# Kernel tuning notes

Measured on AMD Instinct MI355X. Metric: run time of the kernel, lower is better.

## Reference

```python
import jax, jax.numpy as jnp
import numpy as np

N, M, D = 16384, 4096, 128
NEG = -1e30  # masked-score fill


def setup_inputs() -> dict:
    key = jax.random.key(0)
    k1, k2, k3, k4 = jax.random.split(key, 4)
    self_feats = jax.random.normal(k1, (N, D), dtype=jnp.float32)
    features_neighs = jax.random.normal(k2, (M, D), dtype=jnp.float32)
    neigh_matrix = jax.random.randint(k3, (N, M), 0, 2, dtype=jnp.int32)
    # xavier_uniform for a: shape (2D, 1), gain=1 -> limit = sqrt(6/(2D+1))
    limit = float(np.sqrt(6.0 / (2 * D + 1)))
    a = jax.random.uniform(k4, (2 * D, 1), minval=-limit, maxval=limit, dtype=jnp.float32)
    return {"self_feats": self_feats, "features_neighs": features_neighs,
            "neigh_matrix": neigh_matrix, "a": a}


def reference(self_feats, features_neighs, neigh_matrix, a):
    # a = [a_self; a_neigh]; cat([self_i, neigh_j]) @ a = self_i@a_self + neigh_j@a_neigh
    d = self_feats.shape[1]
    s_self = self_feats @ a[:d, 0]        # [N]
    s_neigh = features_neighs @ a[d:, 0]  # [M]
    scores = jax.nn.leaky_relu(s_self[:, None] + s_neigh[None, :], 0.2)  # [N, M]
    mask = neigh_matrix.astype(bool)
    scores = jnp.where(mask, scores, NEG)
    attn = jax.nn.softmax(scores, axis=1)          # masked softmax per node
    attn = jnp.where(mask, attn, 0.0)              # nodes with no neighbors -> zeros
    return attn @ features_neighs                  # [N, D] weighted neighbor sum
```

## Files before the change

### kernel.cpp

```cpp
#include <hip/hip_runtime.h>
#include <hip/hip_bf16.h>

#define NROWS 16384
#define MCOLS 4096
#define DDIM  128
#define LOG2E 1.4426950408889634f

typedef __attribute__((ext_vector_type(8))) short short8;
typedef __attribute__((ext_vector_type(4))) float f32x4;

__device__ __forceinline__ float wave_reduce_add(float d) {
#pragma unroll
  for (int off = 32; off >= 1; off >>= 1) d += __shfl_xor(d, off, 64);
  return d;
}

__device__ __forceinline__ float pcalc(float t, int m) {
  float u = fmaxf(t, 0.2f * t);
  float e = exp2f(u);
  return m != 0 ? e : 0.f;
}

__device__ __forceinline__ unsigned short f2bf(float f) {
  unsigned u = __builtin_bit_cast(unsigned, f);
  return (unsigned short)((u + 0x7fffu + ((u >> 16) & 1u)) >> 16);
}

__device__ __forceinline__ unsigned pack_bf2(float lo, float hi) {
  return (unsigned)f2bf(lo) | ((unsigned)f2bf(hi) << 16);
}

__global__ __launch_bounds__(256) void aggr_prep(
    const float* __restrict__ V, const float* __restrict__ a,
    float* __restrict__ sneigh, short* __restrict__ packedV) {
  const int t = threadIdx.x, lane = t & 63, w = t >> 6;
  const int blk = blockIdx.x;

  float a0 = a[DDIM + 2 * lane] * LOG2E;
  float a1 = a[DDIM + 2 * lane + 1] * LOG2E;
#pragma unroll
  for (int i = 0; i < 4; ++i) {
    int j = blk * 16 + w * 4 + i;
    float2 v = *(const float2*)(V + (long)j * DDIM + 2 * lane);
    float d = wave_reduce_add(v.x * a0 + v.y * a1);
    if (lane == 0) sneigh[j] = d;
  }

  const int tg = blk * 256 + t;
  const int l = tg & 63;
  const int chunkid = tg >> 6;
  const int c = chunkid & 15, kt = chunkid >> 4;
  const int ks2 = c >> 3, cf = c & 7;
  const int col = cf * 16 + (l & 15);
  const long krow = (long)kt * 64 + ks2 * 32 + (l >> 4) * 8;
  short8 o;
#pragma unroll
  for (int b = 0; b < 8; ++b) {
    float f = V[(krow + b) * DDIM + col];
    o[b] = (short)f2bf(f);
  }
  *(short8*)(packedV + (long)tg * 8) = o;
}

__global__ __launch_bounds__(512, 2) void aggr_main(
    const float* __restrict__ self_feats, const int* __restrict__ nm,
    const float* __restrict__ a, const float* __restrict__ sneigh,
    const short* __restrict__ packedV, float* __restrict__ out) {
  __shared__ float s_sn[MCOLS];
  __shared__ float s_ss[64];
  __shared__ __align__(16) short Bst[2][2][8192];
  __shared__ float comb[4][16][132];
  __shared__ float den_x[64];
  __shared__ float den_f[64];

  const int t = threadIdx.x, lane = t & 63, w = t >> 6;
  const int rw = w & 3, ks = w >> 2;
  const int blk = blockIdx.x;
  const int rowblk = blk * 64;
  const int arow = lane & 15, kg = lane >> 4;

  {
    float a0 = a[2 * lane] * LOG2E, a1 = a[2 * lane + 1] * LOG2E;
#pragma unroll
    for (int i = 0; i < 8; ++i) {
      int r = w * 8 + i;
      float2 v = *(const float2*)(self_feats + (long)(rowblk + r) * DDIM + 2 * lane);
      float d = wave_reduce_add(v.x * a0 + v.y * a1);
      if (lane == 0) s_ss[r] = d;
    }
  }
  {
    const float4* src = (const float4*)sneigh;
    float4* dst = (float4*)s_sn;
    dst[t] = src[t];
    dst[t + 512] = src[t + 512];
  }

  auto STAGE = [&](int buf, int it2) {
    int ktn = it2 * 2 + ks;
#pragma unroll
    for (int j = 0; j < 4; ++j) {
      int c = (w & 3) * 4 + j;
      const short* g = packedV + ((long)(ktn * 16 + c) * 64 + lane) * 8;
      __builtin_amdgcn_global_load_lds(
          (const __attribute__((address_space(1))) void*)g,
          (__attribute__((address_space(3))) void*)(&Bst[buf][ks][c * 512]),
          16, 0, 0);
    }
  };

  const int* mbase = nm + (long)(rowblk + rw * 16 + arow) * MCOLS + kg * 8;

  int4 mc[4], mn[4] = {};
  STAGE(0, 0);
  {
    const int kt0 = ks;
#pragma unroll
    for (int ks2 = 0; ks2 < 2; ++ks2)
#pragma unroll
      for (int q = 0; q < 2; ++q)
        mc[ks2 * 2 + q] = *(const int4*)(mbase + kt0 * 64 + ks2 * 32 + q * 4);
  }
  __syncthreads();

  const float si = s_ss[rw * 16 + arow];

  f32x4 acc[8];
#pragma unroll
  for (int i = 0; i < 8; ++i) acc[i] = (f32x4){0.f, 0.f, 0.f, 0.f};
  float den = 0.f;

#pragma unroll 2
  for (int it = 0; it < 32; ++it) {
    const int kt = it * 2 + ks;
    const int buf = it & 1;
    if (it < 31) {
      STAGE(buf ^ 1, it + 1);
      __builtin_amdgcn_sched_barrier(0);
      const int ktn = (it + 1) * 2 + ks;
#pragma unroll
      for (int ks2 = 0; ks2 < 2; ++ks2)
#pragma unroll
        for (int q = 0; q < 2; ++q)
          mn[ks2 * 2 + q] = *(const int4*)(mbase + ktn * 64 + ks2 * 32 + q * 4);
      __builtin_amdgcn_sched_barrier(0);
    }

    short8 afr[2];
#pragma unroll
    for (int ks2 = 0; ks2 < 2; ++ks2) {
      const float* sj = &s_sn[kt * 64 + ks2 * 32 + kg * 8];
      float4 s0 = *(const float4*)sj;
      float4 s1 = *(const float4*)(sj + 4);
      int4 m0 = mc[ks2 * 2], m1 = mc[ks2 * 2 + 1];
      float p0 = pcalc(si + s0.x, m0.x);
      float p1 = pcalc(si + s0.y, m0.y);
      float p2 = pcalc(si + s0.z, m0.z);
      float p3 = pcalc(si + s0.w, m0.w);
      float p4 = pcalc(si + s1.x, m1.x);
      float p5 = pcalc(si + s1.y, m1.y);
      float p6 = pcalc(si + s1.z, m1.z);
      float p7 = pcalc(si + s1.w, m1.w);
      den += ((p0 + p1) + (p2 + p3)) + ((p4 + p5) + (p6 + p7));
      int4 ai;
      ai.x = (int)pack_bf2(p0, p1);
      ai.y = (int)pack_bf2(p2, p3);
      ai.z = (int)pack_bf2(p4, p5);
      ai.w = (int)pack_bf2(p6, p7);
      afr[ks2] = __builtin_bit_cast(short8, ai);
    }

    const short8* Bks = (const short8*)&Bst[buf][ks][0];
#pragma unroll
    for (int cf = 0; cf < 8; ++cf) {
      acc[cf] = __builtin_amdgcn_mfma_f32_16x16x32_bf16(afr[0], Bks[cf * 64 + lane], acc[cf], 0, 0, 0);
      acc[cf] = __builtin_amdgcn_mfma_f32_16x16x32_bf16(afr[1], Bks[(8 + cf) * 64 + lane], acc[cf], 0, 0, 0);
    }

    asm volatile("s_waitcnt vmcnt(4)" ::: "memory");
    __builtin_amdgcn_sched_barrier(0);
    __builtin_amdgcn_s_barrier();
    mc[0] = mn[0]; mc[1] = mn[1]; mc[2] = mn[2]; mc[3] = mn[3];
  }

  den += __shfl_xor(den, 16, 64);
  den += __shfl_xor(den, 32, 64);

  if (ks == 1) {
#pragma unroll
    for (int cf = 0; cf < 8; ++cf)
#pragma unroll
      for (int r = 0; r < 4; ++r)
        comb[rw][kg * 4 + r][cf * 16 + arow] = acc[cf][r];
    if (lane < 16) den_x[rw * 16 + lane] = den;
  }
  __syncthreads();
  if (ks == 0) {
    float dtot = den + den_x[rw * 16 + arow];
    if (lane < 16) den_f[rw * 16 + lane] = dtot;
  }
  __syncthreads();
  if (ks == 0) {
    float rcp[4];
#pragma unroll
    for (int r = 0; r < 4; ++r) {
      float dv = den_f[rw * 16 + kg * 4 + r];
      rcp[r] = dv > 0.f ? 1.0f / dv : 0.f;
    }
#pragma unroll
    for (int cf = 0; cf < 8; ++cf)
#pragma unroll
      for (int r = 0; r < 4; ++r) {
        float v = (acc[cf][r] + comb[rw][kg * 4 + r][cf * 16 + arow]) * rcp[r];
        out[(long)(rowblk + rw * 16 + kg * 4 + r) * DDIM + cf * 16 + arow] = v;
      }
  }
}

extern "C" void kernel_launch(void* const* d_in, const int* in_sizes, int n_in,
                              void* d_out, int out_size, void* d_ws, size_t ws_size,
                              hipStream_t stream) {
  const float* self_feats = (const float*)d_in[0];
  const float* V = (const float*)d_in[1];
  const int* nm = (const int*)d_in[2];
  const float* a = (const float*)d_in[3];
  float* out = (float*)d_out;

  float* sneigh = (float*)d_ws;
  short* packedV = (short*)((char*)d_ws + 16384);

  aggr_prep<<<256, 256, 0, stream>>>(V, a, sneigh, packedV);
  aggr_main<<<256, 512, 0, stream>>>(self_feats, nm, a, sneigh, packedV, out);
}
```

Before: 400.5 us.

## Drop intra-block K split; use four waves each covering full K range

Removes the two-way split of the neighbor dimension across wave groups, so each of four waves processes all 64 K tiles for its 16 rows. This eliminates the LDS combine buffers, two block barriers and the cross-group partial-sum reduction. Block size drops from 512 to 256 threads while the grid stays at 256 blocks. The cost is that each CU has half as many waves issuing mask loads, which lowers memory-level parallelism in a bandwidth/latency bound loop.

```diff
diff --git a/kernel.cpp b/kernel.cpp
--- a/kernel.cpp
+++ b/kernel.cpp
@@ -62,19 +62,15 @@
   *(short8*)(packedV + (long)tg * 8) = o;
 }
 
-__global__ __launch_bounds__(512, 2) void aggr_main(
+__global__ __launch_bounds__(256, 3) void aggr_main(
     const float* __restrict__ self_feats, const int* __restrict__ nm,
     const float* __restrict__ a, const float* __restrict__ sneigh,
     const short* __restrict__ packedV, float* __restrict__ out) {
   __shared__ float s_sn[MCOLS];
   __shared__ float s_ss[64];
-  __shared__ __align__(16) short Bst[2][2][8192];
-  __shared__ float comb[4][16][132];
-  __shared__ float den_x[64];
-  __shared__ float den_f[64];
+  __shared__ __align__(16) short Bst[2][8192];
 
   const int t = threadIdx.x, lane = t & 63, w = t >> 6;
-  const int rw = w & 3, ks = w >> 2;
   const int blk = blockIdx.x;
   const int rowblk = blk * 64;
   const int arow = lane & 15, kg = lane >> 4;
@@ -82,8 +78,8 @@
   {
     float a0 = a[2 * lane] * LOG2E, a1 = a[2 * lane + 1] * LOG2E;
 #pragma unroll
-    for (int i = 0; i < 8; ++i) {
-      int r = w * 8 + i;
+    for (int i = 0; i < 16; ++i) {
+      int r = w * 16 + i;
       float2 v = *(const float2*)(self_feats + (long)(rowblk + r) * DDIM + 2 * lane);
       float d = wave_reduce_add(v.x * a0 + v.y * a1);
       if (lane == 0) s_ss[r] = d;
@@ -93,37 +89,35 @@
     const float4* src = (const float4*)sneigh;
     float4* dst = (float4*)s_sn;
     dst[t] = src[t];
+    dst[t + 256] = src[t + 256];
     dst[t + 512] = src[t + 512];
-  }
-
-  auto STAGE = [&](int buf, int it2) {
-    int ktn = it2 * 2 + ks;
+    dst[t + 768] = src[t + 768];
+  }
+
+  auto STAGE = [&](int buf, int kt) {
 #pragma unroll
     for (int j = 0; j < 4; ++j) {
-      int c = (w & 3) * 4 + j;
-      const short* g = packedV + ((long)(ktn * 16 + c) * 64 + lane) * 8;
+      int c = w * 4 + j;
+      const short* g = packedV + ((long)(kt * 16 + c) * 64 + lane) * 8;
       __builtin_amdgcn_global_load_lds(
           (const __attribute__((address_space(1))) void*)g,
-          (__attribute__((address_space(3))) void*)(&Bst[buf][ks][c * 512]),
+          (__attribute__((address_space(3))) void*)(&Bst[buf][c * 512]),
           16, 0, 0);
     }
   };
 
-  const int* mbase = nm + (long)(rowblk + rw * 16 + arow) * MCOLS + kg * 8;
+  const int* mbase = nm + (long)(rowblk + w * 16 + arow) * MCOLS + kg * 8;
 
   int4 mc[4], mn[4] = {};
   STAGE(0, 0);
-  {
-    const int kt0 = ks;
-#pragma unroll
-    for (int ks2 = 0; ks2 < 2; ++ks2)
-#pragma unroll
-      for (int q = 0; q < 2; ++q)
-        mc[ks2 * 2 + q] = *(const int4*)(mbase + kt0 * 64 + ks2 * 32 + q * 4);
-  }
+#pragma unroll
+  for (int ks2 = 0; ks2 < 2; ++ks2)
+#pragma unroll
+    for (int q = 0; q < 2; ++q)
+      mc[ks2 * 2 + q] = *(const int4*)(mbase + ks2 * 32 + q * 4);
   __syncthreads();
 
-  const float si = s_ss[rw * 16 + arow];
+  const float si = s_ss[w * 16 + arow];
 
   f32x4 acc[8];
 #pragma unroll
@@ -131,25 +125,23 @@
   float den = 0.f;
 
 #pragma unroll 2
-  for (int it = 0; it < 32; ++it) {
-    const int kt = it * 2 + ks;
+  for (int it = 0; it < 64; ++it) {
     const int buf = it & 1;
-    if (it < 31) {
+    if (it < 63) {
       STAGE(buf ^ 1, it + 1);
       __builtin_amdgcn_sched_barrier(0);
-      const int ktn = (it + 1) * 2 + ks;
 #pragma unroll
       for (int ks2 = 0; ks2 < 2; ++ks2)
 #pragma unroll
         for (int q = 0; q < 2; ++q)
-          mn[ks2 * 2 + q] = *(const int4*)(mbase + ktn * 64 + ks2 * 32 + q * 4);
+          mn[ks2 * 2 + q] = *(const int4*)(mbase + (it + 1) * 64 + ks2 * 32 + q * 4);
       __builtin_amdgcn_sched_barrier(0);
     }
 
     short8 afr[2];
 #pragma unroll
     for (int ks2 = 0; ks2 < 2; ++ks2) {
-      const float* sj = &s_sn[kt * 64 + ks2 * 32 + kg * 8];
+      const float* sj = &s_sn[it * 64 + ks2 * 32 + kg * 8];
       float4 s0 = *(const float4*)sj;
       float4 s1 = *(const float4*)(sj + 4);
       int4 m0 = mc[ks2 * 2], m1 = mc[ks2 * 2 + 1];
@@ -170,7 +162,7 @@
       afr[ks2] = __builtin_bit_cast(short8, ai);
     }
 
-    const short8* Bks = (const short8*)&Bst[buf][ks][0];
+    const short8* Bks = (const short8*)&Bst[buf][0];
 #pragma unroll
     for (int cf = 0; cf < 8; ++cf) {
       acc[cf] = __builtin_amdgcn_mfma_f32_16x16x32_bf16(afr[0], Bks[cf * 64 + lane], acc[cf], 0, 0, 0);
@@ -186,35 +178,18 @@
   den += __shfl_xor(den, 16, 64);
   den += __shfl_xor(den, 32, 64);
 
-  if (ks == 1) {
-#pragma unroll
-    for (int cf = 0; cf < 8; ++cf)
-#pragma unroll
-      for (int r = 0; r < 4; ++r)
-        comb[rw][kg * 4 + r][cf * 16 + arow] = acc[cf][r];
-    if (lane < 16) den_x[rw * 16 + lane] = den;
-  }
-  __syncthreads();
-  if (ks == 0) {
-    float dtot = den + den_x[rw * 16 + arow];
-    if (lane < 16) den_f[rw * 16 + lane] = dtot;
-  }
-  __syncthreads();
-  if (ks == 0) {
-    float rcp[4];
-#pragma unroll
-    for (int r = 0; r < 4; ++r) {
-      float dv = den_f[rw * 16 + kg * 4 + r];
-      rcp[r] = dv > 0.f ? 1.0f / dv : 0.f;
-    }
-#pragma unroll
-    for (int cf = 0; cf < 8; ++cf)
-#pragma unroll
-      for (int r = 0; r < 4; ++r) {
-        float v = (acc[cf][r] + comb[rw][kg * 4 + r][cf * 16 + arow]) * rcp[r];
-        out[(long)(rowblk + rw * 16 + kg * 4 + r) * DDIM + cf * 16 + arow] = v;
-      }
-  }
+  float rcp[4];
+#pragma unroll
+  for (int r = 0; r < 4; ++r) {
+    float dv = __shfl(den, kg * 4 + r, 64);
+    rcp[r] = dv > 0.f ? 1.0f / dv : 0.f;
+  }
+#pragma unroll
+  for (int cf = 0; cf < 8; ++cf)
+#pragma unroll
+    for (int r = 0; r < 4; ++r)
+      out[(long)(rowblk + w * 16 + kg * 4 + r) * DDIM + cf * 16 + arow] =
+          acc[cf][r] * rcp[r];
 }
 
 extern "C" void kernel_launch(void* const* d_in, const int* in_sizes, int n_in,
@@ -230,5 +205,5 @@
   short* packedV = (short*)((char*)d_ws + 16384);
 
   aggr_prep<<<256, 256, 0, stream>>>(V, a, sneigh, packedV);
-  aggr_main<<<256, 512, 0, stream>>>(self_feats, nm, a, sneigh, packedV, out);
-}
+  aggr_main<<<256, 256, 0, stream>>>(self_feats, nm, a, sneigh, packedV, out);
+}
```

After: 421.4 us. +5.2%, slower.
